# Optimization experiments

Hardware: AMD Instinct MI355X
Metric: run time of the kernel (lower is better)

Reference implementation:

```python
import jax, jax.numpy as jnp
import numpy as np

B = 65536
NE = 256   # n_encode
NH = 256   # n_hidden
NC = 4     # n_command
D = 64     # n_depth (BatchNorm channels)
F = 32     # n_features
M = D * (F // 2)  # 1024
EPS = 1e-5


def setup_inputs() -> dict:
    key = jax.random.key(0)
    ks = jax.random.split(key, 8)
    s = 0.05
    return {
        "feature": jax.random.normal(ks[0], (B, NE), jnp.float32),
        "hidden":  jax.random.normal(ks[1], (B, NH), jnp.float32),
        "command": jax.random.normal(ks[2], (B, NC), jnp.float32),
        # linear weights (torch Linear stores [out, in]); xavier-like scale
        "Wq":  jax.random.normal(ks[3], (D, NC), jnp.float32) * s,
        "Wkz": jax.random.normal(ks[4], (M, NE), jnp.float32) * s,
        "Wkh": jax.random.normal(ks[5], (M, NH), jnp.float32) * s,
        "Wvz": jax.random.normal(ks[6], (M, NE), jnp.float32) * s,
        "Wvh": jax.random.normal(ks[7], (M, NH), jnp.float32) * s,
        # BatchNorm1d(64) affine params (normV exists in __init__ but is unused)
        "gammaQ": jnp.ones((D,), jnp.float32),
        "betaQ":  jnp.zeros((D,), jnp.float32),
        "gammaK": jnp.ones((D,), jnp.float32),
        "betaK":  jnp.zeros((D,), jnp.float32),
    }


def reference(feature, hidden, command, Wq, Wkz, Wkh, Wvz, Wvh,
              gammaQ, betaQ, gammaK, betaK):
    # Q projection: [B, D]; BatchNorm1d over batch (training-mode batch stats,
    # biased variance, matching torch).
    Q = command @ Wq.T
    mQ = jnp.mean(Q, axis=0)
    vQ = jnp.mean(jnp.square(Q - mQ), axis=0)
    Qn = (Q - mQ) / jnp.sqrt(vQ + EPS) * gammaQ + betaQ          # [B, D]

    # K: cat([B,M],[B,M]) -> [B, 2M] -> view [B, F, D] -> transpose -> [B, D, F]
    K = jnp.concatenate([feature @ Wkz.T, hidden @ Wkh.T], axis=1)
    K = K.reshape(-1, F, D).transpose(0, 2, 1)                    # [B, D, F]
    mK = jnp.mean(K, axis=(0, 2), keepdims=True)
    vK = jnp.mean(jnp.square(K - mK), axis=(0, 2), keepdims=True)
    Kn = (K - mK) / jnp.sqrt(vK + EPS) * gammaK[None, :, None] + betaK[None, :, None]

    # V: [B, F, D], NOT batch-normed (normV is dead code in the original)
    V = jnp.concatenate([feature @ Wvz.T, hidden @ Wvh.T], axis=1).reshape(-1, F, D)

    # attention: [B,1,D] @ [B,D,F] -> [B,F] scores; softmax over F; then @ V
    A = jax.nn.softmax(jnp.einsum('bd,bdf->bf', Qn, Kn) / np.sqrt(D).astype(np.float32), axis=-1)
    s = jnp.einsum('bf,bfd->bd', A, V)                            # [B, D]
    return s
```

## Files before the change

kernel.cpp:

```cpp
#include <hip/hip_runtime.h>
#include <hip/hip_bf16.h>
#include <math.h>


typedef float  f32x4   __attribute__((ext_vector_type(4)));
typedef float  f32x16  __attribute__((ext_vector_type(16)));
typedef __bf16 bf16x4  __attribute__((ext_vector_type(4)));
typedef __bf16 bf16x8  __attribute__((ext_vector_type(8)));

#define MFMA16(A, B, C) __builtin_amdgcn_mfma_f32_16x16x32_bf16((A), (B), (C), 0, 0, 0)
#define MFMA32(A, B, C) __builtin_amdgcn_mfma_f32_32x32x16_bf16((A), (B), (C), 0, 0, 0)

#define EPSV 1e-5f

#define WS_WV    0x000000u
#define WS_WKF   0x100000u
#define WS_G     0x120000u
#define WS_CS    0x1A0000u
#define WS_CMDP  0x1A0800u
#define WS_T     0x1A1800u
#define WS_U     0x1A3800u

__device__ __forceinline__ void gl_lds16(const void* g, void* l)
{
    __builtin_amdgcn_global_load_lds(
        (const __attribute__((address_space(1))) unsigned int*)g,
        (__attribute__((address_space(3))) unsigned int*)l, 16, 0, 0);
}

__global__ __launch_bounds__(512, 2) void setup1(const float* __restrict__ feat,
        const float* __restrict__ hid, const float4* __restrict__ cmd,
        const float* __restrict__ Wvz, const float* __restrict__ Wvh,
        __bf16* __restrict__ WV, float* __restrict__ CMDP, float* __restrict__ CS,
        __bf16* __restrict__ Gp)
{
    __shared__ __bf16 T[2 * 256 * 40];
    __shared__ float sm[8][14];
    const int blk = blockIdx.x;
    const int tid = threadIdx.x;

    if (blk >= 384) {
        const int b2 = blk - 384;
        float v[14];
#pragma unroll
        for (int k = 0; k < 14; ++k) v[k] = 0.f;
#pragma unroll
        for (int i = 0; i < 4; ++i) {
            float4 c = cmd[(b2 * 4 + i) * 512 + tid];
            v[0] += c.x;  v[1] += c.y;  v[2] += c.z;  v[3] += c.w;
            v[4] += c.x*c.x; v[5] += c.x*c.y; v[6] += c.x*c.z; v[7] += c.x*c.w;
            v[8] += c.y*c.y; v[9] += c.y*c.z; v[10] += c.y*c.w;
            v[11] += c.z*c.z; v[12] += c.z*c.w; v[13] += c.w*c.w;
        }
#pragma unroll
        for (int k = 0; k < 14; ++k) {
            float s = v[k];
#pragma unroll
            for (int off = 32; off; off >>= 1) s += __shfl_xor(s, off);
            if ((tid & 63) == 0) sm[tid >> 6][k] = s;
        }
        __syncthreads();
        if (tid < 14) {
            float s = 0.f;
#pragma unroll
            for (int w = 0; w < 8; ++w) s += sm[w][tid];
            CMDP[b2 * 14 + tid] = s;
        }
        return;
    }
    if (blk >= 128) {
        int t = (blk - 128) * 512 + tid;
        int e = t * 4;
        const float* src = (e < 262144) ? (Wvz + e) : (Wvh + (e - 262144));
        float4 a = *(const float4*)src;
        bf16x4 vv = { (__bf16)a.x, (__bf16)a.y, (__bf16)a.z, (__bf16)a.w };
        *(bf16x4*)(WV + e) = vv;
        return;
    }

    const int mat  = blk >> 6;
    const int chunk = blk & 63;
    const float* X = mat ? hid : feat;
    float* cs = CS + mat * 256;
    const int k0   = chunk * 1024;
    const int wid  = tid >> 6, lane = tid & 63, quad = lane >> 4, l15 = lane & 15;
    const int c    = tid & 255;
    const int t8   = tid >> 8;

    f32x4 acc[2][16];
#pragma unroll
    for (int mt = 0; mt < 2; ++mt)
#pragma unroll
        for (int nt = 0; nt < 16; ++nt) acc[mt][nt] = (f32x4){0.f, 0.f, 0.f, 0.f};

    const float* Xc = X + (size_t)k0 * 256 + c + (size_t)t8 * 16 * 256;
    float ra[16], rb[16];
    float clsum = 0.f;

#define GRAM_LOAD(R, IT) do { \
        const float* p_ = Xc + (size_t)(IT) * 32 * 256; \
        _Pragma("unroll") \
        for (int i_ = 0; i_ < 16; ++i_) (R)[i_] = p_[(size_t)i_ * 256]; \
    } while (0)
#define GRAM_WRITE(R, BUFO) do { \
        _Pragma("unroll") \
        for (int i2_ = 0; i2_ < 4; ++i2_) { \
            float x0_ = (R)[4*i2_], x1_ = (R)[4*i2_+1]; \
            float x2_ = (R)[4*i2_+2], x3_ = (R)[4*i2_+3]; \
            clsum += x0_ + x1_ + x2_ + x3_; \
            bf16x4 v_ = { (__bf16)x0_, (__bf16)x1_, (__bf16)x2_, (__bf16)x3_ }; \
            *(bf16x4*)&T[(BUFO) + c * 40 + t8 * 16 + i2_ * 4] = v_; } \
    } while (0)
#define GRAM_MFMA(BUFO) do { \
        const __bf16* Tb_ = &T[(BUFO)]; \
        bf16x8 a0_ = *(const bf16x8*)&Tb_[(wid * 32 +      l15) * 40 + quad * 8]; \
        bf16x8 a1_ = *(const bf16x8*)&Tb_[(wid * 32 + 16 + l15) * 40 + quad * 8]; \
        _Pragma("unroll") \
        for (int nt_ = 0; nt_ < 16; ++nt_) { \
            bf16x8 b_ = *(const bf16x8*)&Tb_[(nt_ * 16 + l15) * 40 + quad * 8]; \
            acc[0][nt_] = MFMA16(a0_, b_, acc[0][nt_]); \
            acc[1][nt_] = MFMA16(a1_, b_, acc[1][nt_]); } \
    } while (0)

    GRAM_LOAD(ra, 0);
    GRAM_LOAD(rb, 1);
    GRAM_WRITE(ra, 0);
    GRAM_LOAD(ra, 2);
    __syncthreads();

    for (int it2 = 0; it2 < 16; ++it2) {
        GRAM_WRITE(rb, 10240);
        if (it2 < 15) GRAM_LOAD(rb, 2 * it2 + 3);
        GRAM_MFMA(0);
        __syncthreads();
        if (it2 < 15) {
            GRAM_WRITE(ra, 0);
            if (it2 < 14) GRAM_LOAD(ra, 2 * it2 + 4);
        }
        GRAM_MFMA(10240);
        __syncthreads();
    }
#undef GRAM_LOAD
#undef GRAM_WRITE
#undef GRAM_MFMA

    atomicAdd(&cs[c], clsum);
    __bf16* outp = Gp + (size_t)blk * 65536;
#pragma unroll
    for (int mt = 0; mt < 2; ++mt)
#pragma unroll
        for (int nt = 0; nt < 16; ++nt)
#pragma unroll
            for (int r = 0; r < 4; ++r) {
                int gi = wid * 32 + mt * 16 + quad * 4 + r;
                int gj = nt * 16 + l15;
                outp[gi * 256 + gj] = (__bf16)acc[mt][nt][r];
            }
}

__global__ void gram_reduce(const __bf16* __restrict__ Gp, float* __restrict__ G)
{
    int o = blockIdx.x * 256 + threadIdx.x;
    int mat = o >> 16, e = o & 65535;
    const __bf16* p = Gp + (size_t)mat * 64 * 65536 + e;
    float s = 0.f;
#pragma unroll 8
    for (int c = 0; c < 64; ++c) s += (float)p[(size_t)c * 65536];
    G[o] = s;
}

__global__ void rowstats(const float* __restrict__ Wkz, const float* __restrict__ Wkh,
        const float* __restrict__ G, const float* __restrict__ CS,
        float* __restrict__ Tout, float* __restrict__ Uout)
{
    const int blk = blockIdx.x;
    const int mat = blk >> 7, jg = blk & 127;
    const float* Wsrc = (mat ? Wkh : Wkz) + (size_t)jg * 8 * 256;
    const float* Gm = G + (size_t)mat * 65536;
    const float* cs = CS + mat * 256;
    __shared__ float wlT[256 * 8];
    __shared__ float red[4][16];
    const int tid = threadIdx.x, wid = tid >> 6, lane = tid & 63;
#pragma unroll
    for (int jj = 0; jj < 8; ++jj) wlT[tid * 8 + jj] = Wsrc[jj * 256 + tid];
    __syncthreads();
    float inner[8];
#pragma unroll
    for (int jj = 0; jj < 8; ++jj) inner[jj] = 0.f;
    for (int r = 0; r < 256; ++r) {
        float g = Gm[r * 256 + tid];
        float4 w0 = *(const float4*)&wlT[r * 8];
        float4 w1 = *(const float4*)&wlT[r * 8 + 4];
        inner[0] = fmaf(w0.x, g, inner[0]); inner[1] = fmaf(w0.y, g, inner[1]);
        inner[2] = fmaf(w0.z, g, inner[2]); inner[3] = fmaf(w0.w, g, inner[3]);
        inner[4] = fmaf(w1.x, g, inner[4]); inner[5] = fmaf(w1.y, g, inner[5]);
        inner[6] = fmaf(w1.z, g, inner[6]); inner[7] = fmaf(w1.w, g, inner[7]);
    }
    float cst = cs[tid];
#pragma unroll
    for (int jj = 0; jj < 8; ++jj) {
        float wme = wlT[tid * 8 + jj];
        float p = wme * inner[jj];
        float u = wme * cst;
#pragma unroll
        for (int off = 32; off; off >>= 1) { p += __shfl_xor(p, off); u += __shfl_xor(u, off); }
        if (lane == 0) { red[wid][jj] = p; red[wid][jj + 8] = u; }
    }
    __syncthreads();
    if (tid < 16) {
        float s = red[0][tid] + red[1][tid] + red[2][tid] + red[3][tid];
        int jj = tid & 7;
        int j = mat * 1024 + jg * 8 + jj;
        if (tid < 8) Tout[j] = s; else Uout[j] = s;
    }
}

__global__ void foldK(const float* __restrict__ Wkz, const float* __restrict__ Wkh,
                      const float* __restrict__ Wq,
                      const float* __restrict__ gQ, const float* __restrict__ bQ,
                      const float* __restrict__ gK, const float* __restrict__ bK,
                      const float* __restrict__ CMDP, const float* __restrict__ T,
                      const float* __restrict__ U, __bf16* __restrict__ WKF)
{
    __shared__ float s14[14];
    __shared__ float sC0[64];
    __shared__ float sWq2[256];
    const int tid = threadIdx.x;
    if (tid < 14) {
        float s = 0.f;
        for (int b = 0; b < 32; ++b) s += CMDP[b * 14 + tid];
        s14[tid] = s;
    }
    __syncthreads();
    if (tid < 64) {
        const int d = tid;
        float s4[4] = { s14[0], s14[1], s14[2], s14[3] };
        float gc[4][4];
        gc[0][0] = s14[4];
        gc[0][1] = gc[1][0] = s14[5];
        gc[0][2] = gc[2][0] = s14[6];
        gc[0][3] = gc[3][0] = s14[7];
        gc[1][1] = s14[8];
        gc[1][2] = gc[2][1] = s14[9];
        gc[1][3] = gc[3][1] = s14[10];
        gc[2][2] = s14[11];
        gc[2][3] = gc[3][2] = s14[12];
        gc[3][3] = s14[13];
        float wq[4];
#pragma unroll
        for (int c = 0; c < 4; ++c) wq[c] = Wq[d * 4 + c];
        const float invB = 1.0f / 65536.0f;
        float mQ = (wq[0]*s4[0] + wq[1]*s4[1] + wq[2]*s4[2] + wq[3]*s4[3]) * invB;
        float eq2 = 0.f;
#pragma unroll
        for (int c = 0; c < 4; ++c)
#pragma unroll
            for (int c2 = 0; c2 < 4; ++c2) eq2 += wq[c] * wq[c2] * gc[c][c2];
        eq2 *= invB;
        float vQ  = eq2 - mQ * mQ;
        float aQ  = gQ[d] / sqrtf(vQ + EPSV);
        float bQv = bQ[d] - mQ * aQ;
        float S2 = 0.f, S1 = 0.f;
#pragma unroll
        for (int f = 0; f < 32; ++f) { S2 += T[f * 64 + d]; S1 += U[f * 64 + d]; }
        const float invBF = 1.0f / (65536.0f * 32.0f);
        float e2 = S2 * invBF, mK = S1 * invBF;
        float vK = e2 - mK * mK;
        float aK = gK[d] / sqrtf(vK + EPSV);
        float c1 = aQ * aK * 0.125f;
        sC0[d] = bQv * aK * 0.125f;
#pragma unroll
        for (int c = 0; c < 4; ++c) sWq2[d * 4 + c] = c1 * wq[c];
    }
    __syncthreads();

    const int blk = blockIdx.x;
    const int h = blk / 96, rr = blk % 96;
    const int k = tid;
    float s = 0.f;
    if (rr < 80) {
        const int c = rr >> 4, fl = rr & 15;
        const float* Wsrc = (h ? Wkh : Wkz) + (size_t)fl * 64 * 256;
        for (int d = 0; d < 64; ++d) {
            float coef = (c == 0) ? sC0[d] : sWq2[d * 4 + (c - 1)];
            s = fmaf(coef, Wsrc[d * 256 + k], s);
        }
    }
    WKF[(size_t)(h * 96 + rr) * 256 + k] = (__bf16)s;
}

__global__ __launch_bounds__(256, 2) void fused_attn(
        const float* __restrict__ feat, const float* __restrict__ hid,
        const float4* __restrict__ cmd, const __bf16* __restrict__ WV,
        const __bf16* __restrict__ WKF, float* __restrict__ out)
{
    __shared__ __bf16 BUF[32768];
    __shared__ __bf16 WGTs[16 * 132];
    const int tid  = threadIdx.x;
    const int wid  = tid >> 6, lane = tid & 63;
    const int l5   = lane & 31, hi = lane >> 5;
    const int fl   = l5 & 15;
    const bool low = (l5 < 16);
    const int wrow = (blockIdx.x << 7) + (wid << 5);

#define STAGE_CHUNK(SRC, DSTBASE, I) do { \
        int n_ = (wid << 1) + ((I) << 3) + hi; \
        gl_lds16((SRC) + n_ * 256 + ((l5 ^ (n_ & 31)) << 3), \
                 &BUF[(DSTBASE) + (((wid << 1) + ((I) << 3)) << 8)]); \
    } while (0)

    float l_i[16];
    f32x16 s_acc[2];
#pragma unroll
    for (int r = 0; r < 16; ++r) { l_i[r] = 0.f; s_acc[0][r] = 0.f; s_acc[1][r] = 0.f; }

    for (int h = 0; h < 2; ++h) {
        const float* X = h ? hid : feat;
        const __bf16* Wkf = WKF + ((size_t)h * 96 << 8);

        __syncthreads();
#pragma unroll
        for (int i = 0; i < 12; ++i)
            STAGE_CHUNK(Wkf, 0, i);

        bf16x8 a2[16];
#pragma unroll
        for (int u = 0; u < 16; ++u) {
            const float* p = X + ((size_t)(wrow + l5) << 8) + u * 16 + hi * 8;
            float4 x0 = *(const float4*)p;
            float4 x1 = *(const float4*)(p + 4);
            a2[u] = (bf16x8){ (__bf16)x0.x, (__bf16)x0.y, (__bf16)x0.z, (__bf16)x0.w,
                              (__bf16)x1.x, (__bf16)x1.y, (__bf16)x1.z, (__bf16)x1.w };
        }
        __syncthreads();

        f32x16 acc1[3];
#pragma unroll
        for (int nt = 0; nt < 3; ++nt)
#pragma unroll
            for (int r = 0; r < 16; ++r) acc1[nt][r] = 0.f;
        __builtin_amdgcn_s_setprio(1);
#pragma unroll
        for (int ks = 0; ks < 16; ++ks)
#pragma unroll
            for (int nt = 0; nt < 3; ++nt) {
                int n = nt * 32 + l5;
                bf16x8 b = *(const bf16x8*)&BUF[n * 256 + (((ks * 2 + hi) ^ (n & 31)) << 3)];
                acc1[nt] = MFMA32(a2[ks], b, acc1[nt]);
            }
        __builtin_amdgcn_s_setprio(0);

#pragma unroll
        for (int g = 0; g < 4; ++g) {
            bf16x4 wv4;
#pragma unroll
            for (int j = 0; j < 4; ++j) {
                const int r = g * 4 + j;
                const int row32 = j + 8 * g + 4 * hi;
                float4 cm = cmd[wrow + row32];
                float e0, e1, t0[3], t1[3];
#pragma unroll
                for (int nt = 0; nt < 3; ++nt) {
                    e0 = acc1[nt][r];
                    e1 = __shfl_xor(e0, 16);
                    t0[nt] = low ? e0 : e1;
                    t1[nt] = low ? e1 : e0;
                }
                float sc = t0[0] + cm.x * t1[0] + cm.y * t0[1]
                                 + cm.z * t1[1] + cm.w * t0[2];
                float w = __expf(sc);
                wv4[j] = (__bf16)w;
                float ws = w;
                ws += __shfl_xor(ws, 1); ws += __shfl_xor(ws, 2);
                ws += __shfl_xor(ws, 4); ws += __shfl_xor(ws, 8);
                l_i[r] += ws;
            }
            if (low) *(bf16x4*)&WGTs[fl * 132 + (wid << 5) + 8 * g + 4 * hi] = wv4;
        }

        __syncthreads();

        {
            const __bf16* base = WV + ((size_t)(h * 16) << 14);
#pragma unroll
            for (int i = 0; i < 8; ++i)
                STAGE_CHUNK(base, 0, i);
        }

        for (int f2 = 0; f2 < 16; ++f2) {
            const int bufsel = (f2 & 1) << 14;
            if (f2 < 15) {
                const __bf16* base = WV + ((size_t)(h * 16 + f2 + 1) << 14);
                const int nsel = bufsel ^ 16384;
#pragma unroll
                for (int i = 0; i < 8; ++i)
                    STAGE_CHUNK(base, nsel, i);
                asm volatile("s_waitcnt vmcnt(8)");
            } else {
                asm volatile("s_waitcnt vmcnt(0)");
            }
            __builtin_amdgcn_sched_barrier(0);
            __builtin_amdgcn_s_barrier();
            __builtin_amdgcn_sched_barrier(0);

            f32x16 acc2[2];
#pragma unroll
            for (int r = 0; r < 16; ++r) { acc2[0][r] = 0.f; acc2[1][r] = 0.f; }
            __builtin_amdgcn_s_setprio(1);
#pragma unroll
            for (int ks = 0; ks < 16; ++ks)
#pragma unroll
                for (int nt = 0; nt < 2; ++nt) {
                    int n = nt * 32 + l5;
                    bf16x8 b = *(const bf16x8*)&BUF[bufsel + n * 256
                                                    + (((ks * 2 + hi) ^ (n & 31)) << 3)];
                    acc2[nt] = MFMA32(a2[ks], b, acc2[nt]);
                }
            __builtin_amdgcn_s_setprio(0);
#pragma unroll
            for (int g = 0; g < 4; ++g) {
                bf16x4 wv = *(const bf16x4*)&WGTs[f2 * 132 + (wid << 5) + 8 * g + 4 * hi];
#pragma unroll
                for (int j = 0; j < 4; ++j) {
                    float w = (float)wv[j];
                    s_acc[0][g * 4 + j] += w * acc2[0][g * 4 + j];
                    s_acc[1][g * 4 + j] += w * acc2[1][g * 4 + j];
                }
            }
            __builtin_amdgcn_sched_barrier(0);
            __builtin_amdgcn_s_barrier();
            __builtin_amdgcn_sched_barrier(0);
        }
    }
#undef STAGE_CHUNK

#pragma unroll
    for (int g = 0; g < 4; ++g)
#pragma unroll
        for (int j = 0; j < 4; ++j) {
            const int r = g * 4 + j;
            float inv = 1.0f / l_i[r];
            size_t row = (size_t)(wrow + j + 8 * g + 4 * hi);
            out[(row << 6) + l5]      = s_acc[0][r] * inv;
            out[(row << 6) + 32 + l5] = s_acc[1][r] * inv;
        }
}

extern "C" void kernel_launch(void* const* d_in, const int* in_sizes, int n_in,
                              void* d_out, int out_size, void* d_ws, size_t ws_size,
                              hipStream_t stream)
{
    (void)in_sizes; (void)n_in; (void)out_size; (void)ws_size;
    const float* feature = (const float*)d_in[0];
    const float* hidden  = (const float*)d_in[1];
    const float* command = (const float*)d_in[2];
    const float* Wq      = (const float*)d_in[3];
    const float* Wkz     = (const float*)d_in[4];
    const float* Wkh     = (const float*)d_in[5];
    const float* Wvz     = (const float*)d_in[6];
    const float* Wvh     = (const float*)d_in[7];
    const float* gammaQ  = (const float*)d_in[8];
    const float* betaQ   = (const float*)d_in[9];
    const float* gammaK  = (const float*)d_in[10];
    const float* betaK   = (const float*)d_in[11];

    char* ws = (char*)d_ws;
    __bf16* WV   = (__bf16*)(ws + WS_WV);
    __bf16* WKF  = (__bf16*)(ws + WS_WKF);
    float*  G    = (float*)(ws + WS_G);
    float*  CS   = (float*)(ws + WS_CS);
    float*  CMDP = (float*)(ws + WS_CMDP);
    float*  Tj   = (float*)(ws + WS_T);
    float*  Uj   = (float*)(ws + WS_U);
    float*  outp = (float*)d_out;
    __bf16* Gp   = (__bf16*)d_out;

    hipMemsetAsync(ws + WS_CS, 0, 0x800, stream);
    setup1<<<416, 512, 0, stream>>>(feature, hidden, (const float4*)command,
                                    Wvz, Wvh, WV, CMDP, CS, Gp);
    gram_reduce<<<512, 256, 0, stream>>>(Gp, G);
    rowstats<<<256, 256, 0, stream>>>(Wkz, Wkh, G, CS, Tj, Uj);
    foldK<<<192, 256, 0, stream>>>(Wkz, Wkh, Wq, gammaQ, betaQ, gammaK, betaK,
                                   CMDP, Tj, Uj, WKF);
    fused_attn<<<512, 256, 0, stream>>>(feature, hidden, (const float4*)command,
                                        WV, WKF, outp);
}
```

Baseline: 322.8 us.

## Process two 32-row M tiles per wave with half the waves per block

```diff
diff --git a/kernel.cpp b/kernel.cpp
--- a/kernel.cpp
+++ b/kernel.cpp
@@ -289,7 +289,7 @@
     WKF[(size_t)(h * 96 + rr) * 256 + k] = (__bf16)s;
 }
 
-__global__ __launch_bounds__(256, 2) void fused_attn(
+__global__ __launch_bounds__(128, 1) void fused_attn(
         const float* __restrict__ feat, const float* __restrict__ hid,
         const float4* __restrict__ cmd, const __bf16* __restrict__ WV,
         const __bf16* __restrict__ WKF, float* __restrict__ out)
@@ -301,18 +301,22 @@
     const int l5   = lane & 31, hi = lane >> 5;
     const int fl   = l5 & 15;
     const bool low = (l5 < 16);
-    const int wrow = (blockIdx.x << 7) + (wid << 5);
+    const int wrow = (blockIdx.x << 7) + (wid << 6);
 
 #define STAGE_CHUNK(SRC, DSTBASE, I) do { \
-        int n_ = (wid << 1) + ((I) << 3) + hi; \
+        int n_ = (wid << 1) + ((I) << 2) + hi; \
         gl_lds16((SRC) + n_ * 256 + ((l5 ^ (n_ & 31)) << 3), \
-                 &BUF[(DSTBASE) + (((wid << 1) + ((I) << 3)) << 8)]); \
+                 &BUF[(DSTBASE) + (((wid << 1) + ((I) << 2)) << 8)]); \
     } while (0)
 
-    float l_i[16];
-    f32x16 s_acc[2];
-#pragma unroll
-    for (int r = 0; r < 16; ++r) { l_i[r] = 0.f; s_acc[0][r] = 0.f; s_acc[1][r] = 0.f; }
+    float l_i[2][16];
+    f32x16 s_acc[2][2];
+#pragma unroll
+    for (int m = 0; m < 2; ++m)
+#pragma unroll
+        for (int r = 0; r < 16; ++r) {
+            l_i[m][r] = 0.f; s_acc[m][0][r] = 0.f; s_acc[m][1][r] = 0.f;
+        }
 
     for (int h = 0; h < 2; ++h) {
         const float* X = h ? hid : feat;
@@ -320,25 +324,29 @@
 
         __syncthreads();
 #pragma unroll
-        for (int i = 0; i < 12; ++i)
+        for (int i = 0; i < 24; ++i)
             STAGE_CHUNK(Wkf, 0, i);
 
-        bf16x8 a2[16];
-#pragma unroll
-        for (int u = 0; u < 16; ++u) {
-            const float* p = X + ((size_t)(wrow + l5) << 8) + u * 16 + hi * 8;
-            float4 x0 = *(const float4*)p;
-            float4 x1 = *(const float4*)(p + 4);
-            a2[u] = (bf16x8){ (__bf16)x0.x, (__bf16)x0.y, (__bf16)x0.z, (__bf16)x0.w,
-                              (__bf16)x1.x, (__bf16)x1.y, (__bf16)x1.z, (__bf16)x1.w };
-        }
+        bf16x8 a2[2][16];
+#pragma unroll
+        for (int m = 0; m < 2; ++m)
+#pragma unroll
+            for (int u = 0; u < 16; ++u) {
+                const float* p = X + ((size_t)(wrow + m * 32 + l5) << 8) + u * 16 + hi * 8;
+                float4 x0 = *(const float4*)p;
+                float4 x1 = *(const float4*)(p + 4);
+                a2[m][u] = (bf16x8){ (__bf16)x0.x, (__bf16)x0.y, (__bf16)x0.z, (__bf16)x0.w,
+                                     (__bf16)x1.x, (__bf16)x1.y, (__bf16)x1.z, (__bf16)x1.w };
+            }
         __syncthreads();
 
-        f32x16 acc1[3];
-#pragma unroll
-        for (int nt = 0; nt < 3; ++nt)
-#pragma unroll
-            for (int r = 0; r < 16; ++r) acc1[nt][r] = 0.f;
+        f32x16 acc1[2][3];
+#pragma unroll
+        for (int m = 0; m < 2; ++m)
+#pragma unroll
+            for (int nt = 0; nt < 3; ++nt)
+#pragma unroll
+                for (int r = 0; r < 16; ++r) acc1[m][nt][r] = 0.f;
         __builtin_amdgcn_s_setprio(1);
 #pragma unroll
         for (int ks = 0; ks < 16; ++ks)
@@ -346,44 +354,48 @@
             for (int nt = 0; nt < 3; ++nt) {
                 int n = nt * 32 + l5;
                 bf16x8 b = *(const bf16x8*)&BUF[n * 256 + (((ks * 2 + hi) ^ (n & 31)) << 3)];
-                acc1[nt] = MFMA32(a2[ks], b, acc1[nt]);
+                acc1[0][nt] = MFMA32(a2[0][ks], b, acc1[0][nt]);
+                acc1[1][nt] = MFMA32(a2[1][ks], b, acc1[1][nt]);
             }
         __builtin_amdgcn_s_setprio(0);
 
 #pragma unroll
-        for (int g = 0; g < 4; ++g) {
-            bf16x4 wv4;
-#pragma unroll
-            for (int j = 0; j < 4; ++j) {
-                const int r = g * 4 + j;
-                const int row32 = j + 8 * g + 4 * hi;
-                float4 cm = cmd[wrow + row32];
-                float e0, e1, t0[3], t1[3];
-#pragma unroll
-                for (int nt = 0; nt < 3; ++nt) {
-                    e0 = acc1[nt][r];
-                    e1 = __shfl_xor(e0, 16);
-                    t0[nt] = low ? e0 : e1;
-                    t1[nt] = low ? e1 : e0;
+        for (int m = 0; m < 2; ++m)
+#pragma unroll
+            for (int g = 0; g < 4; ++g) {
+                bf16x4 wv4;
+#pragma unroll
+                for (int j = 0; j < 4; ++j) {
+                    const int r = g * 4 + j;
+                    const int row32 = j + 8 * g + 4 * hi;
+                    float4 cm = cmd[wrow + m * 32 + row32];
+                    float e0, e1, t0[3], t1[3];
+#pragma unroll
+                    for (int nt = 0; nt < 3; ++nt) {
+                        e0 = acc1[m][nt][r];
+                        e1 = __shfl_xor(e0, 16);
+                        t0[nt] = low ? e0 : e1;
+                        t1[nt] = low ? e1 : e0;
+                    }
+                    float sc = t0[0] + cm.x * t1[0] + cm.y * t0[1]
+                                     + cm.z * t1[1] + cm.w * t0[2];
+                    float w = __expf(sc);
+                    wv4[j] = (__bf16)w;
+                    float ws = w;
+                    ws += __shfl_xor(ws, 1); ws += __shfl_xor(ws, 2);
+                    ws += __shfl_xor(ws, 4); ws += __shfl_xor(ws, 8);
+                    l_i[m][r] += ws;
                 }
-                float sc = t0[0] + cm.x * t1[0] + cm.y * t0[1]
-                                 + cm.z * t1[1] + cm.w * t0[2];
-                float w = __expf(sc);
-                wv4[j] = (__bf16)w;
-                float ws = w;
-                ws += __shfl_xor(ws, 1); ws += __shfl_xor(ws, 2);
-                ws += __shfl_xor(ws, 4); ws += __shfl_xor(ws, 8);
-                l_i[r] += ws;
+                if (low) *(bf16x4*)&WGTs[fl * 132 + (wid << 6) + (m << 5)
+                                         + 8 * g + 4 * hi] = wv4;
             }
-            if (low) *(bf16x4*)&WGTs[fl * 132 + (wid << 5) + 8 * g + 4 * hi] = wv4;
-        }
 
         __syncthreads();
 
         {
             const __bf16* base = WV + ((size_t)(h * 16) << 14);
 #pragma unroll
-            for (int i = 0; i < 8; ++i)
+            for (int i = 0; i < 16; ++i)
                 STAGE_CHUNK(base, 0, i);
         }
 
@@ -393,9 +405,9 @@
                 const __bf16* base = WV + ((size_t)(h * 16 + f2 + 1) << 14);
                 const int nsel = bufsel ^ 16384;
 #pragma unroll
-                for (int i = 0; i < 8; ++i)
+                for (int i = 0; i < 16; ++i)
                     STAGE_CHUNK(base, nsel, i);
-                asm volatile("s_waitcnt vmcnt(8)");
+                asm volatile("s_waitcnt vmcnt(16)");
             } else {
                 asm volatile("s_waitcnt vmcnt(0)");
             }
@@ -403,9 +415,11 @@
             __builtin_amdgcn_s_barrier();
             __builtin_amdgcn_sched_barrier(0);
 
-            f32x16 acc2[2];
-#pragma unroll
-            for (int r = 0; r < 16; ++r) { acc2[0][r] = 0.f; acc2[1][r] = 0.f; }
+            f32x16 acc2[2][2];
+#pragma unroll
+            for (int m = 0; m < 2; ++m)
+#pragma unroll
+                for (int r = 0; r < 16; ++r) { acc2[m][0][r] = 0.f; acc2[m][1][r] = 0.f; }
             __builtin_amdgcn_s_setprio(1);
 #pragma unroll
             for (int ks = 0; ks < 16; ++ks)
@@ -414,19 +428,23 @@
                     int n = nt * 32 + l5;
                     bf16x8 b = *(const bf16x8*)&BUF[bufsel + n * 256
                                                     + (((ks * 2 + hi) ^ (n & 31)) << 3)];
-                    acc2[nt] = MFMA32(a2[ks], b, acc2[nt]);
+                    acc2[0][nt] = MFMA32(a2[0][ks], b, acc2[0][nt]);
+                    acc2[1][nt] = MFMA32(a2[1][ks], b, acc2[1][nt]);
                 }
             __builtin_amdgcn_s_setprio(0);
 #pragma unroll
-            for (int g = 0; g < 4; ++g) {
-                bf16x4 wv = *(const bf16x4*)&WGTs[f2 * 132 + (wid << 5) + 8 * g + 4 * hi];
-#pragma unroll
-                for (int j = 0; j < 4; ++j) {
-                    float w = (float)wv[j];
-                    s_acc[0][g * 4 + j] += w * acc2[0][g * 4 + j];
-                    s_acc[1][g * 4 + j] += w * acc2[1][g * 4 + j];
+            for (int m = 0; m < 2; ++m)
+#pragma unroll
+                for (int g = 0; g < 4; ++g) {
+                    bf16x4 wv = *(const bf16x4*)&WGTs[f2 * 132 + (wid << 6) + (m << 5)
+                                                      + 8 * g + 4 * hi];
+#pragma unroll
+                    for (int j = 0; j < 4; ++j) {
+                        float w = (float)wv[j];
+                        s_acc[m][0][g * 4 + j] += w * acc2[m][0][g * 4 + j];
+                        s_acc[m][1][g * 4 + j] += w * acc2[m][1][g * 4 + j];
+                    }
                 }
-            }
             __builtin_amdgcn_sched_barrier(0);
             __builtin_amdgcn_s_barrier();
             __builtin_amdgcn_sched_barrier(0);
@@ -435,15 +453,17 @@
 #undef STAGE_CHUNK
 
 #pragma unroll
-    for (int g = 0; g < 4; ++g)
-#pragma unroll
-        for (int j = 0; j < 4; ++j) {
-            const int r = g * 4 + j;
-            float inv = 1.0f / l_i[r];
-            size_t row = (size_t)(wrow + j + 8 * g + 4 * hi);
-            out[(row << 6) + l5]      = s_acc[0][r] * inv;
-            out[(row << 6) + 32 + l5] = s_acc[1][r] * inv;
-        }
+    for (int m = 0; m < 2; ++m)
+#pragma unroll
+        for (int g = 0; g < 4; ++g)
+#pragma unroll
+            for (int j = 0; j < 4; ++j) {
+                const int r = g * 4 + j;
+                float inv = 1.0f / l_i[m][r];
+                size_t row = (size_t)(wrow + m * 32 + j + 8 * g + 4 * hi);
+                out[(row << 6) + l5]      = s_acc[m][0][r] * inv;
+                out[(row << 6) + 32 + l5] = s_acc[m][1][r] * inv;
+            }
 }
 
 extern "C" void kernel_launch(void* const* d_in, const int* in_sizes, int n_in,
@@ -482,6 +502,6 @@
     rowstats<<<256, 256, 0, stream>>>(Wkz, Wkh, G, CS, Tj, Uj);
     foldK<<<192, 256, 0, stream>>>(Wkz, Wkh, Wq, gammaQ, betaQ, gammaK, betaK,
                                    CMDP, Tj, Uj, WKF);
-    fused_attn<<<512, 256, 0, stream>>>(feature, hidden, (const float4*)command,
+    fused_attn<<<512, 128, 0, stream>>>(feature, hidden, (const float4*)command,
                                         WV, WKF, outp);
 }
```

Result: slower. 377.8 us (+17.0%).
